# Kernel tuning notes

Hardware: AMD Instinct MI355X
Metric: run time of the kernel (lower is better)

## Reference

```python
import jax, jax.numpy as jnp
import numpy as np
from jax import lax

EMBED_DIM = 384
NUM_GROUPS = 128
GROUP_SIZE = 64
LN_EPS = 1e-5


def setup_inputs() -> dict:
    key = jax.random.key(0)
    k_pts, k1, k2, k3, k4 = jax.random.split(key, 5)
    B, N = 32, 16384
    points = jax.random.normal(k_pts, (B, N, 3), dtype=jnp.float32)
    # local_mlp: Linear(3,128) -> GELU -> Linear(128, embed_dim)
    w1 = jax.random.normal(k1, (3, 128), dtype=jnp.float32) * (1.0 / np.sqrt(3))
    b1 = jax.random.normal(k2, (128,), dtype=jnp.float32) * 0.01
    w2 = jax.random.normal(k3, (128, EMBED_DIM), dtype=jnp.float32) * (1.0 / np.sqrt(128))
    b2 = jax.random.normal(k4, (EMBED_DIM,), dtype=jnp.float32) * 0.01
    ln_scale = jnp.ones((EMBED_DIM,), dtype=jnp.float32)
    ln_bias = jnp.zeros((EMBED_DIM,), dtype=jnp.float32)
    return {"points": points, "w1": w1, "b1": b1, "w2": w2, "b2": b2,
            "ln_scale": ln_scale, "ln_bias": ln_bias}


def _farthest_point_sample(points, num_samples):
    # points: [B, N, 3]. Deterministic start at index 0 (torch uses randint).
    B, N, _ = points.shape

    def step(carry, _):
        distance, farthest = carry  # [B, N], [B]
        centroid = jnp.take_along_axis(points, farthest[:, None, None], axis=1)  # [B,1,3]
        d = jnp.sum((points - centroid) ** 2, axis=-1)  # [B, N]
        distance = jnp.minimum(distance, d)
        nxt = jnp.argmax(distance, axis=-1).astype(jnp.int32)
        return (distance, nxt), farthest

    init = (jnp.full((B, N), jnp.inf, dtype=points.dtype),
            jnp.zeros((B,), dtype=jnp.int32))
    _, idx = lax.scan(step, init, None, length=num_samples)  # [S, B]
    return idx.T  # [B, S]


def reference(points, w1, b1, w2, b2, ln_scale, ln_bias):
    B, N, _ = points.shape
    centroid_idx = _farthest_point_sample(points, NUM_GROUPS)  # [B, G]
    centroids = jnp.take_along_axis(
        points, centroid_idx[:, :, None].astype(jnp.int32), axis=1)  # [B, G, 3]

    # squared distances (same ordering as torch.cdist for topk); matmul form
    # avoids materializing a [B, G, N, 3] diff tensor.
    c2 = jnp.sum(centroids ** 2, axis=-1)  # [B, G]
    p2 = jnp.sum(points ** 2, axis=-1)     # [B, N]
    dist2 = c2[:, :, None] + p2[:, None, :] - 2.0 * jnp.einsum(
        'bgc,bnc->bgn', centroids, points)  # [B, G, N]

    # k smallest -> top_k of negated distances
    _, neighbor_idx = lax.top_k(-dist2, GROUP_SIZE)  # [B, G, K]

    batch_ix = jnp.arange(B)[:, None, None]
    grouped = points[batch_ix, neighbor_idx]  # [B, G, K, 3]
    local_coords = grouped - centroids[:, :, None, :]  # [B, G, K, 3]

    h = jax.nn.gelu(local_coords @ w1 + b1, approximate=False)  # [B,G,K,128]
    feats = h @ w2 + b2  # [B, G, K, D]
    tokens = jnp.mean(feats, axis=2)  # [B, G, D]

    mu = jnp.mean(tokens, axis=-1, keepdims=True)
    var = jnp.mean((tokens - mu) ** 2, axis=-1, keepdims=True)
    tokens_ln = (tokens - mu) * lax.rsqrt(var + LN_EPS) * ln_scale + ln_bias
    return centroids, tokens_ln
```

## Files before the change

### kernel.cpp

```cpp
#include <hip/hip_runtime.h>
#include <math.h>

#define BB 32
#define NN 16384
#define GG 128
#define KK 64
#define HH 128
#define DD 384
#define LN_EPS 1e-5f
#define NBUCK 2048
#define CANDCAP 1024

__device__ __forceinline__ float sq3(float x, float y, float z) {
    return __fadd_rn(__fadd_rn(__fmul_rn(x, x), __fmul_rn(y, y)), __fmul_rn(z, z));
}

__device__ __forceinline__ unsigned distkey(float px, float py, float pz, float4 c4) {
    float p2 = sq3(px, py, pz);
    float dot = __fadd_rn(__fadd_rn(__fmul_rn(c4.x, px), __fmul_rn(c4.y, py)),
                          __fmul_rn(c4.z, pz));
    float d = __fsub_rn(__fadd_rn(c4.w, p2), __fmul_rn(2.0f, dot));
    unsigned u = __float_as_uint(d);
    return u ^ ((u & 0x80000000u) ? 0xFFFFFFFFu : 0x80000000u);
}

__global__ void prep_kernel(const float* __restrict__ w2, float* __restrict__ w2t) {
    int i = blockIdx.x * 256 + threadIdx.x;
    if (i < HH * DD) {
        int f = i >> 7;
        int k = i & 127;
        w2t[i] = w2[k * DD + f];
    }
}

__global__ __launch_bounds__(512, 2) void fps_kernel(const float* __restrict__ pts,
                                                     float* __restrict__ cent_out,
                                                     float4* __restrict__ cent_pad) {
    const int b = blockIdx.x;
    const int tid = threadIdx.x;
    const float* p = pts + (size_t)b * NN * 3;
    const float4* p4 = (const float4*)p;

    float x[32], y[32], z[32], dist[32];
#pragma unroll
    for (int j = 0; j < 8; j++) {
        int q = j * 512 + tid;
        float4 A = p4[3 * q], B = p4[3 * q + 1], C = p4[3 * q + 2];
        x[j * 4 + 0] = A.x; y[j * 4 + 0] = A.y; z[j * 4 + 0] = A.z;
        x[j * 4 + 1] = A.w; y[j * 4 + 1] = B.x; z[j * 4 + 1] = B.y;
        x[j * 4 + 2] = B.z; y[j * 4 + 2] = B.w; z[j * 4 + 2] = C.x;
        x[j * 4 + 3] = C.y; y[j * 4 + 3] = C.z; z[j * 4 + 3] = C.w;
#pragma unroll
        for (int t = 0; t < 4; t++) dist[j * 4 + t] = INFINITY;
    }

    __shared__ unsigned long long slot[GG];
    for (int i = tid; i < GG; i += 512) slot[i] = 0ull;
    __syncthreads();

    float cx = p[0], cy = p[1], cz = p[2];

    for (int it = 0; it < GG; it++) {
        if (tid == 0) {
            float* co = cent_out + ((size_t)b * GG + it) * 3;
            co[0] = cx; co[1] = cy; co[2] = cz;
            cent_pad[b * GG + it] = make_float4(cx, cy, cz, sq3(cx, cy, cz));
        }
        if (it == GG - 1) break;

        float bv0 = -INFINITY, bv1 = -INFINITY, bv2 = -INFINITY, bv3 = -INFINITY;
        int bi0 = 0, bi1 = 0, bi2 = 0, bi3 = 0;
#pragma unroll
        for (int j = 0; j < 8; j++) {
            int nb = 4 * (j * 512 + tid);
#pragma unroll
            for (int t = 0; t < 4; t++) {
                int r = j * 4 + t;
                float dx = __fsub_rn(x[r], cx);
                float dy = __fsub_rn(y[r], cy);
                float dz = __fsub_rn(z[r], cz);
                float d = sq3(dx, dy, dz);
                float dj = fminf(dist[r], d);
                dist[r] = dj;
                int n = nb + t;
                switch (t) {
                    case 0: if (dj > bv0) { bv0 = dj; bi0 = n; } break;
                    case 1: if (dj > bv1) { bv1 = dj; bi1 = n; } break;
                    case 2: if (dj > bv2) { bv2 = dj; bi2 = n; } break;
                    case 3: if (dj > bv3) { bv3 = dj; bi3 = n; } break;
                }
            }
        }
        float fv = bv0; int fi = bi0;
        if (bv1 > fv || (bv1 == fv && bi1 < fi)) { fv = bv1; fi = bi1; }
        if (bv2 > fv || (bv2 == fv && bi2 < fi)) { fv = bv2; fi = bi2; }
        if (bv3 > fv || (bv3 == fv && bi3 < fi)) { fv = bv3; fi = bi3; }
#pragma unroll
        for (int off = 32; off >= 1; off >>= 1) {
            float ov = __shfl_down(fv, off);
            int oi = __shfl_down(fi, off);
            if (ov > fv || (ov == fv && oi < fi)) { fv = ov; fi = oi; }
        }
        if ((tid & 63) == 0) {
            unsigned long long packed =
                ((unsigned long long)__float_as_uint(fv) << 32) |
                (unsigned)(0xFFFFFFFFu - (unsigned)fi);
            atomicMax(&slot[it], packed);
        }
        __syncthreads();
        unsigned long long w = slot[it];
        int idx = (int)(0xFFFFFFFFu - (unsigned)w);
        const float* wp = p + (size_t)idx * 3;
        cx = wp[0]; cy = wp[1]; cz = wp[2];
    }
}

__global__ __launch_bounds__(256, 6) void group_kernel(
    const float* __restrict__ pts, const float4* __restrict__ cent_pad,
    const float* __restrict__ w1, const float* __restrict__ b1,
    const float* __restrict__ w2t, const float* __restrict__ b2,
    const float* __restrict__ lns, const float* __restrict__ lnb,
    float* __restrict__ tok_out) {
    __shared__ __align__(16) union {
        unsigned hist[NBUCK];
        unsigned long long cand[CANDCAP];
    } sh;
    __shared__ int selIdx[KK];
    __shared__ float4 localPt[KK];
    __shared__ float w1s[3 * HH];
    __shared__ float b1s[HH];
    __shared__ __align__(16) float hbar[HH];
    __shared__ float partial[256];
    __shared__ float red2[8];
    __shared__ float toks[DD];
    __shared__ int waveSum[4];
    __shared__ unsigned long long wmin[4];
    __shared__ unsigned TA_S;
    __shared__ int cntS;
    __shared__ unsigned long long lastS;
    __shared__ float muS, rstdS;

    const int tid = threadIdx.x;
    int bid = blockIdx.x;
    int xcd = bid & 7, sub = bid >> 3;
    int b = xcd * 4 + (sub >> 7);
    int g = sub & 127;

    const float* p = pts + (size_t)b * NN * 3;
    const float4* p4 = (const float4*)p;
    float4 c4 = cent_pad[b * GG + g];

    for (int i = tid; i < 3 * HH; i += 256) w1s[i] = w1[i];
    if (tid < HH) b1s[tid] = b1[tid];
    for (int i = tid; i < NBUCK; i += 256) sh.hist[i] = 0;
    if (tid == 0) cntS = 0;
    __syncthreads();

    for (int i = 0; i < 16; i++) {
        int t4 = i * 256 + tid;
        float4 A = p4[3 * t4], B = p4[3 * t4 + 1], C = p4[3 * t4 + 2];
        unsigned k0 = distkey(A.x, A.y, A.z, c4);
        unsigned k1 = distkey(A.w, B.x, B.y, c4);
        unsigned k2 = distkey(B.z, B.w, C.x, c4);
        unsigned k3 = distkey(C.y, C.z, C.w, c4);
        atomicAdd(&sh.hist[k0 >> 21], 1u);
        atomicAdd(&sh.hist[k1 >> 21], 1u);
        atomicAdd(&sh.hist[k2 >> 21], 1u);
        atomicAdd(&sh.hist[k3 >> 21], 1u);
    }
    __syncthreads();

    {
        uint4 h0 = ((const uint4*)sh.hist)[tid * 2];
        uint4 h1 = ((const uint4*)sh.hist)[tid * 2 + 1];
        int loc[8] = {(int)h0.x, (int)h0.y, (int)h0.z, (int)h0.w,
                      (int)h1.x, (int)h1.y, (int)h1.z, (int)h1.w};
        int s = 0;
#pragma unroll
        for (int j = 0; j < 8; j++) s += loc[j];
        int lane = tid & 63, wid = tid >> 6;
        int v = s;
#pragma unroll
        for (int off = 1; off < 64; off <<= 1) {
            int o = __shfl_up(v, off);
            if (lane >= off) v += o;
        }
        if (lane == 63) waveSum[wid] = v;
        __syncthreads();
        int base = 0;
        for (int w = 0; w < wid; w++) base += waveSum[w];
        int c = base + v - s;
#pragma unroll
        for (int j = 0; j < 8; j++) {
            if (c < KK && c + loc[j] >= KK) TA_S = (unsigned)(tid * 8 + j);
            c += loc[j];
        }
        __syncthreads();
    }
    unsigned TA = TA_S;

    for (int i = 0; i < 16; i++) {
        int t4 = i * 256 + tid;
        float4 A = p4[3 * t4], B = p4[3 * t4 + 1], C = p4[3 * t4 + 2];
        unsigned k[4];
        k[0] = distkey(A.x, A.y, A.z, c4);
        k[1] = distkey(A.w, B.x, B.y, c4);
        k[2] = distkey(B.z, B.w, C.x, c4);
        k[3] = distkey(C.y, C.z, C.w, c4);
#pragma unroll
        for (int q = 0; q < 4; q++) {
            if ((k[q] >> 21) <= TA) {
                int pos = atomicAdd(&cntS, 1);
                if (pos < CANDCAP)
                    sh.cand[pos] =
                        ((unsigned long long)k[q] << 32) | (unsigned)(4 * t4 + q);
            }
        }
    }
    __syncthreads();
    int cnt = cntS;

    if (cnt <= CANDCAP) {
        for (int c0 = tid; c0 < cnt; c0 += 256) {
            unsigned long long pr = sh.cand[c0];
            int rank = 0;
            int j = 0;
            for (; j + 8 <= cnt; j += 8) {
                unsigned long long a0 = sh.cand[j + 0];
                unsigned long long a1 = sh.cand[j + 1];
                unsigned long long a2 = sh.cand[j + 2];
                unsigned long long a3 = sh.cand[j + 3];
                unsigned long long a4 = sh.cand[j + 4];
                unsigned long long a5 = sh.cand[j + 5];
                unsigned long long a6 = sh.cand[j + 6];
                unsigned long long a7 = sh.cand[j + 7];
                rank += (int)(a0 < pr) + (int)(a1 < pr) + (int)(a2 < pr) +
                        (int)(a3 < pr) + (int)(a4 < pr) + (int)(a5 < pr) +
                        (int)(a6 < pr) + (int)(a7 < pr);
            }
            for (; j < cnt; j++) rank += (int)(sh.cand[j] < pr);
            if (rank < KK) selIdx[rank] = (int)(unsigned)pr;
        }
        __syncthreads();
    } else {
        if (tid == 0) lastS = 0ull;
        __syncthreads();
        for (int r = 0; r < KK; r++) {
            unsigned long long last = lastS;
            unsigned long long best = 0xFFFFFFFFFFFFFFFFull;
            for (int i = 0; i < 16; i++) {
                int t4 = i * 256 + tid;
                float4 A = p4[3 * t4], B = p4[3 * t4 + 1], C = p4[3 * t4 + 2];
                unsigned k[4];
                k[0] = distkey(A.x, A.y, A.z, c4);
                k[1] = distkey(A.w, B.x, B.y, c4);
                k[2] = distkey(B.z, B.w, C.x, c4);
                k[3] = distkey(C.y, C.z, C.w, c4);
#pragma unroll
                for (int q = 0; q < 4; q++) {
                    unsigned long long pr =
                        ((unsigned long long)k[q] << 32) | (unsigned)(4 * t4 + q);
                    if ((r == 0 || pr > last) && pr < best) best = pr;
                }
            }
            unsigned blo = (unsigned)best, bhi = (unsigned)(best >> 32);
#pragma unroll
            for (int off = 32; off >= 1; off >>= 1) {
                unsigned olo = __shfl_down(blo, off);
                unsigned ohi = __shfl_down(bhi, off);
                unsigned long long ob = ((unsigned long long)ohi << 32) | olo;
                unsigned long long cur = ((unsigned long long)bhi << 32) | blo;
                if (ob < cur) { blo = olo; bhi = ohi; }
            }
            int lane = tid & 63, wid = tid >> 6;
            if (lane == 0) wmin[wid] = ((unsigned long long)bhi << 32) | blo;
            __syncthreads();
            if (tid == 0) {
                unsigned long long m = wmin[0];
                for (int w = 1; w < 4; w++) if (wmin[w] < m) m = wmin[w];
                selIdx[r] = (int)(unsigned)m;
                lastS = m;
            }
            __syncthreads();
        }
    }

    if (tid < KK) {
        int n = selIdx[tid];
        float px = p[n * 3], py = p[n * 3 + 1], pz = p[n * 3 + 2];
        localPt[tid] = make_float4(px - c4.x, py - c4.y, pz - c4.z, 0.f);
    }
    __syncthreads();
    {
        int f = tid & 127, half = tid >> 7;
        float wa = w1s[f], wb = w1s[HH + f], wc = w1s[2 * HH + f], bb = b1s[f];
        float s = 0.f;
        for (int k = half * 32; k < half * 32 + 32; k++) {
            float4 lp = localPt[k];
            float a = lp.x * wa + lp.y * wb + lp.z * wc + bb;
            float hh = 0.5f * a * (1.0f + erff(a * 0.70710678118654752440f));
            s += hh;
        }
        partial[tid] = s;
    }
    __syncthreads();
    if (tid < HH) hbar[tid] = (partial[tid] + partial[tid + HH]) * (1.0f / 64.0f);
    __syncthreads();
    for (int f2 = tid; f2 < DD; f2 += 256) {
        const float4* wrow = (const float4*)(w2t + f2 * HH);
        const float4* hb = (const float4*)hbar;
        float acc = b2[f2];
#pragma unroll 8
        for (int q = 0; q < 32; q++) {
            float4 w4 = wrow[q];
            float4 h4 = hb[q];
            acc += h4.x * w4.x + h4.y * w4.y + h4.z * w4.z + h4.w * w4.w;
        }
        toks[f2] = acc;
    }
    __syncthreads();
    {
        float s1 = 0.f, s2 = 0.f;
        for (int f2 = tid; f2 < DD; f2 += 256) {
            float v = toks[f2];
            s1 += v;
            s2 += v * v;
        }
#pragma unroll
        for (int off = 32; off >= 1; off >>= 1) {
            s1 += __shfl_down(s1, off);
            s2 += __shfl_down(s2, off);
        }
        int lane = tid & 63, wid = tid >> 6;
        if (lane == 0) { partial[wid] = s1; red2[wid] = s2; }
        __syncthreads();
        if (tid == 0) {
            float t1 = partial[0] + partial[1] + partial[2] + partial[3];
            float t2 = red2[0] + red2[1] + red2[2] + red2[3];
            float mu = t1 / (float)DD;
            float var = t2 / (float)DD - mu * mu;
            muS = mu;
            rstdS = rsqrtf(var + LN_EPS);
        }
        __syncthreads();
    }
    float mu = muS, rstd = rstdS;
    float* outp = tok_out + ((size_t)b * GG + g) * DD;
    for (int f2 = tid; f2 < DD; f2 += 256) {
        outp[f2] = (toks[f2] - mu) * rstd * lns[f2] + lnb[f2];
    }
}

extern "C" void kernel_launch(void* const* d_in, const int* in_sizes, int n_in,
                              void* d_out, int out_size, void* d_ws, size_t ws_size,
                              hipStream_t stream) {
    const float* pts = (const float*)d_in[0];
    const float* w1 = (const float*)d_in[1];
    const float* b1 = (const float*)d_in[2];
    const float* w2 = (const float*)d_in[3];
    const float* b2 = (const float*)d_in[4];
    const float* lns = (const float*)d_in[5];
    const float* lnb = (const float*)d_in[6];
    float* out = (float*)d_out;

    float4* cent_pad = (float4*)d_ws;
    float* w2t = (float*)((char*)d_ws + BB * GG * sizeof(float4));

    prep_kernel<<<192, 256, 0, stream>>>(w2, w2t);
    fps_kernel<<<BB, 512, 0, stream>>>(pts, out, cent_pad);
    group_kernel<<<BB * GG, 256, 0, stream>>>(pts, cent_pad, w1, b1, w2t, b2, lns, lnb,
                                              out + BB * GG * 3);
}
```

Before: 533.1 us.

## Precompute padded float4 points with squared norm; wave-aggregate candidate atomics

```diff
diff --git a/kernel.cpp b/kernel.cpp
--- a/kernel.cpp
+++ b/kernel.cpp
@@ -24,6 +24,14 @@
     return u ^ ((u & 0x80000000u) ? 0xFFFFFFFFu : 0x80000000u);
 }
 
+__device__ __forceinline__ unsigned distkey4(float4 p4v, float4 c4) {
+    float dot = __fadd_rn(__fadd_rn(__fmul_rn(c4.x, p4v.x), __fmul_rn(c4.y, p4v.y)),
+                          __fmul_rn(c4.z, p4v.z));
+    float d = __fsub_rn(__fadd_rn(c4.w, p4v.w), __fmul_rn(2.0f, dot));
+    unsigned u = __float_as_uint(d);
+    return u ^ ((u & 0x80000000u) ? 0xFFFFFFFFu : 0x80000000u);
+}
+
 __global__ void prep_kernel(const float* __restrict__ w2, float* __restrict__ w2t) {
     int i = blockIdx.x * 256 + threadIdx.x;
     if (i < HH * DD) {
@@ -31,6 +39,16 @@
         int k = i & 127;
         w2t[i] = w2[k * DD + f];
     }
+}
+
+__global__ void prep_pts4(const float* __restrict__ pts, float4* __restrict__ pts4) {
+    int q = blockIdx.x * 256 + threadIdx.x;
+    const float4* p4 = (const float4*)pts;
+    float4 A = p4[3 * q], B = p4[3 * q + 1], C = p4[3 * q + 2];
+    pts4[4 * q + 0] = make_float4(A.x, A.y, A.z, sq3(A.x, A.y, A.z));
+    pts4[4 * q + 1] = make_float4(A.w, B.x, B.y, sq3(A.w, B.x, B.y));
+    pts4[4 * q + 2] = make_float4(B.z, B.w, C.x, sq3(B.z, B.w, C.x));
+    pts4[4 * q + 3] = make_float4(C.y, C.z, C.w, sq3(C.y, C.z, C.w));
 }
 
 __global__ __launch_bounds__(512, 2) void fps_kernel(const float* __restrict__ pts,
@@ -115,12 +133,13 @@
     }
 }
 
-__global__ __launch_bounds__(256, 6) void group_kernel(
-    const float* __restrict__ pts, const float4* __restrict__ cent_pad,
-    const float* __restrict__ w1, const float* __restrict__ b1,
-    const float* __restrict__ w2t, const float* __restrict__ b2,
-    const float* __restrict__ lns, const float* __restrict__ lnb,
-    float* __restrict__ tok_out) {
+template <int SRC>
+__device__ __forceinline__ void group_body(
+    const float* __restrict__ pts, const float4* __restrict__ pts4,
+    const float4* __restrict__ cent_pad, const float* __restrict__ w1,
+    const float* __restrict__ b1, const float* __restrict__ w2t,
+    const float* __restrict__ b2, const float* __restrict__ lns,
+    const float* __restrict__ lnb, float* __restrict__ tok_out) {
     __shared__ __align__(16) union {
         unsigned hist[NBUCK];
         unsigned long long cand[CANDCAP];
@@ -148,6 +167,7 @@
 
     const float* p = pts + (size_t)b * NN * 3;
     const float4* p4 = (const float4*)p;
+    const float4* pp = pts4 + (size_t)b * NN;
     float4 c4 = cent_pad[b * GG + g];
 
     for (int i = tid; i < 3 * HH; i += 256) w1s[i] = w1[i];
@@ -156,13 +176,24 @@
     if (tid == 0) cntS = 0;
     __syncthreads();
 
+    const int lane = tid & 63, wid = tid >> 6;
+
     for (int i = 0; i < 16; i++) {
         int t4 = i * 256 + tid;
-        float4 A = p4[3 * t4], B = p4[3 * t4 + 1], C = p4[3 * t4 + 2];
-        unsigned k0 = distkey(A.x, A.y, A.z, c4);
-        unsigned k1 = distkey(A.w, B.x, B.y, c4);
-        unsigned k2 = distkey(B.z, B.w, C.x, c4);
-        unsigned k3 = distkey(C.y, C.z, C.w, c4);
+        unsigned k0, k1, k2, k3;
+        if (SRC) {
+            int nb = 4 * t4;
+            k0 = distkey4(pp[nb + 0], c4);
+            k1 = distkey4(pp[nb + 1], c4);
+            k2 = distkey4(pp[nb + 2], c4);
+            k3 = distkey4(pp[nb + 3], c4);
+        } else {
+            float4 A = p4[3 * t4], B = p4[3 * t4 + 1], C = p4[3 * t4 + 2];
+            k0 = distkey(A.x, A.y, A.z, c4);
+            k1 = distkey(A.w, B.x, B.y, c4);
+            k2 = distkey(B.z, B.w, C.x, c4);
+            k3 = distkey(C.y, C.z, C.w, c4);
+        }
         atomicAdd(&sh.hist[k0 >> 21], 1u);
         atomicAdd(&sh.hist[k1 >> 21], 1u);
         atomicAdd(&sh.hist[k2 >> 21], 1u);
@@ -178,7 +209,6 @@
         int s = 0;
 #pragma unroll
         for (int j = 0; j < 8; j++) s += loc[j];
-        int lane = tid & 63, wid = tid >> 6;
         int v = s;
 #pragma unroll
         for (int off = 1; off < 64; off <<= 1) {
@@ -201,19 +231,35 @@
 
     for (int i = 0; i < 16; i++) {
         int t4 = i * 256 + tid;
-        float4 A = p4[3 * t4], B = p4[3 * t4 + 1], C = p4[3 * t4 + 2];
         unsigned k[4];
-        k[0] = distkey(A.x, A.y, A.z, c4);
-        k[1] = distkey(A.w, B.x, B.y, c4);
-        k[2] = distkey(B.z, B.w, C.x, c4);
-        k[3] = distkey(C.y, C.z, C.w, c4);
+        if (SRC) {
+            int nb = 4 * t4;
+            k[0] = distkey4(pp[nb + 0], c4);
+            k[1] = distkey4(pp[nb + 1], c4);
+            k[2] = distkey4(pp[nb + 2], c4);
+            k[3] = distkey4(pp[nb + 3], c4);
+        } else {
+            float4 A = p4[3 * t4], B = p4[3 * t4 + 1], C = p4[3 * t4 + 2];
+            k[0] = distkey(A.x, A.y, A.z, c4);
+            k[1] = distkey(A.w, B.x, B.y, c4);
+            k[2] = distkey(B.z, B.w, C.x, c4);
+            k[3] = distkey(C.y, C.z, C.w, c4);
+        }
 #pragma unroll
         for (int q = 0; q < 4; q++) {
-            if ((k[q] >> 21) <= TA) {
-                int pos = atomicAdd(&cntS, 1);
-                if (pos < CANDCAP)
-                    sh.cand[pos] =
-                        ((unsigned long long)k[q] << 32) | (unsigned)(4 * t4 + q);
+            bool take = (k[q] >> 21) <= TA;
+            unsigned long long m = __ballot(take);
+            if (m != 0ull) {
+                int cw = __popcll(m);
+                int base = 0;
+                if (lane == 0) base = atomicAdd(&cntS, cw);
+                base = __shfl(base, 0);
+                if (take) {
+                    int pos = base + __popcll(m & ((1ull << lane) - 1ull));
+                    if (pos < CANDCAP)
+                        sh.cand[pos] =
+                            ((unsigned long long)k[q] << 32) | (unsigned)(4 * t4 + q);
+                }
             }
         }
     }
@@ -250,12 +296,20 @@
             unsigned long long best = 0xFFFFFFFFFFFFFFFFull;
             for (int i = 0; i < 16; i++) {
                 int t4 = i * 256 + tid;
-                float4 A = p4[3 * t4], B = p4[3 * t4 + 1], C = p4[3 * t4 + 2];
                 unsigned k[4];
-                k[0] = distkey(A.x, A.y, A.z, c4);
-                k[1] = distkey(A.w, B.x, B.y, c4);
-                k[2] = distkey(B.z, B.w, C.x, c4);
-                k[3] = distkey(C.y, C.z, C.w, c4);
+                if (SRC) {
+                    int nb = 4 * t4;
+                    k[0] = distkey4(pp[nb + 0], c4);
+                    k[1] = distkey4(pp[nb + 1], c4);
+                    k[2] = distkey4(pp[nb + 2], c4);
+                    k[3] = distkey4(pp[nb + 3], c4);
+                } else {
+                    float4 A = p4[3 * t4], B = p4[3 * t4 + 1], C = p4[3 * t4 + 2];
+                    k[0] = distkey(A.x, A.y, A.z, c4);
+                    k[1] = distkey(A.w, B.x, B.y, c4);
+                    k[2] = distkey(B.z, B.w, C.x, c4);
+                    k[3] = distkey(C.y, C.z, C.w, c4);
+                }
 #pragma unroll
                 for (int q = 0; q < 4; q++) {
                     unsigned long long pr =
@@ -272,7 +326,6 @@
                 unsigned long long cur = ((unsigned long long)bhi << 32) | blo;
                 if (ob < cur) { blo = olo; bhi = ohi; }
             }
-            int lane = tid & 63, wid = tid >> 6;
             if (lane == 0) wmin[wid] = ((unsigned long long)bhi << 32) | blo;
             __syncthreads();
             if (tid == 0) {
@@ -287,7 +340,13 @@
 
     if (tid < KK) {
         int n = selIdx[tid];
-        float px = p[n * 3], py = p[n * 3 + 1], pz = p[n * 3 + 2];
+        float px, py, pz;
+        if (SRC) {
+            float4 v = pp[n];
+            px = v.x; py = v.y; pz = v.z;
+        } else {
+            px = p[n * 3]; py = p[n * 3 + 1]; pz = p[n * 3 + 2];
+        }
         localPt[tid] = make_float4(px - c4.x, py - c4.y, pz - c4.z, 0.f);
     }
     __syncthreads();
@@ -331,7 +390,6 @@
             s1 += __shfl_down(s1, off);
             s2 += __shfl_down(s2, off);
         }
-        int lane = tid & 63, wid = tid >> 6;
         if (lane == 0) { partial[wid] = s1; red2[wid] = s2; }
         __syncthreads();
         if (tid == 0) {
@@ -349,6 +407,25 @@
     for (int f2 = tid; f2 < DD; f2 += 256) {
         outp[f2] = (toks[f2] - mu) * rstd * lns[f2] + lnb[f2];
     }
+}
+
+__global__ __launch_bounds__(256, 6) void group_kernel_v2(
+    const float* __restrict__ pts, const float4* __restrict__ pts4,
+    const float4* __restrict__ cent_pad, const float* __restrict__ w1,
+    const float* __restrict__ b1, const float* __restrict__ w2t,
+    const float* __restrict__ b2, const float* __restrict__ lns,
+    const float* __restrict__ lnb, float* __restrict__ tok_out) {
+    group_body<1>(pts, pts4, cent_pad, w1, b1, w2t, b2, lns, lnb, tok_out);
+}
+
+__global__ __launch_bounds__(256, 6) void group_kernel_v1(
+    const float* __restrict__ pts, const float4* __restrict__ cent_pad,
+    const float* __restrict__ w1, const float* __restrict__ b1,
+    const float* __restrict__ w2t, const float* __restrict__ b2,
+    const float* __restrict__ lns, const float* __restrict__ lnb,
+    float* __restrict__ tok_out) {
+    group_body<0>(pts, (const float4*)pts, cent_pad, w1, b1, w2t, b2, lns, lnb,
+                  tok_out);
 }
 
 extern "C" void kernel_launch(void* const* d_in, const int* in_sizes, int n_in,
@@ -364,10 +441,19 @@
     float* out = (float*)d_out;
 
     float4* cent_pad = (float4*)d_ws;
-    float* w2t = (float*)((char*)d_ws + BB * GG * sizeof(float4));
+    float* w2t = (float*)((char*)d_ws + 64 * 1024);
+    float4* pts4 = (float4*)((char*)d_ws + 256 * 1024);
+    size_t need = 256 * 1024 + (size_t)BB * NN * sizeof(float4);
 
     prep_kernel<<<192, 256, 0, stream>>>(w2, w2t);
-    fps_kernel<<<BB, 512, 0, stream>>>(pts, out, cent_pad);
-    group_kernel<<<BB * GG, 256, 0, stream>>>(pts, cent_pad, w1, b1, w2t, b2, lns, lnb,
-                                              out + BB * GG * 3);
-}
+    if (ws_size >= need) {
+        prep_pts4<<<(BB * NN / 4) / 256, 256, 0, stream>>>(pts, pts4);
+        fps_kernel<<<BB, 512, 0, stream>>>(pts, out, cent_pad);
+        group_kernel_v2<<<BB * GG, 256, 0, stream>>>(pts, pts4, cent_pad, w1, b1, w2t,
+                                                     b2, lns, lnb, out + BB * GG * 3);
+    } else {
+        fps_kernel<<<BB, 512, 0, stream>>>(pts, out, cent_pad);
+        group_kernel_v1<<<BB * GG, 256, 0, stream>>>(pts, cent_pad, w1, b1, w2t, b2,
+                                                     lns, lnb, out + BB * GG * 3);
+    }
+}
```

New measurement: 576.8 us. 8.2% more time.
